# Performance work log

Hardware: AMD Instinct MI355X
Metric: run time of the kernel (lower is better)

Reference implementation:

```python
import jax, jax.numpy as jnp
import numpy as np

GRID_SIZE = 5
SPLINE_ORDER = 3
GRID_RANGE = (-1.0, 1.0)
EPS = 1e-8


def _make_grid():
    h = (GRID_RANGE[1] - GRID_RANGE[0]) / GRID_SIZE
    # knots: [-spline_order, ..., grid_size + spline_order] * h + lo  -> 12 values
    return jnp.arange(-SPLINE_ORDER, GRID_SIZE + SPLINE_ORDER + 1, dtype=jnp.float32) * h + GRID_RANGE[0]


def _bspline_basis(x, grid):
    # x: [N, in]  ->  bases: [N, in, num_basis] with num_basis = grid_size + spline_order
    xe = x[..., None]                                   # [N, in, 1]
    bases = ((xe >= grid[:-1]) & (xe < grid[1:])).astype(x.dtype)  # [N, in, 11]
    for k in range(1, SPLINE_ORDER + 1):
        left = (xe - grid[: -(k + 1)]) / (grid[k:-1] - grid[: -(k + 1)] + EPS) * bases[..., :-1]
        right = (grid[k + 1:] - xe) / (grid[k + 1:] - grid[1:-k] + EPS) * bases[..., 1:]
        bases = left + right
    return bases                                        # [N, in, 8]


def setup_inputs() -> dict:
    key = jax.random.key(0)
    k1, k2, k3 = jax.random.split(key, 3)
    in_f, out_f, num_basis = 1024, 1024, GRID_SIZE + SPLINE_ORDER
    N = 4096
    x = jax.random.normal(k1, (N, in_f), dtype=jnp.float32)
    base_weight = jax.random.normal(k2, (out_f, in_f), dtype=jnp.float32) * (1.0 / np.sqrt(in_f))
    base_bias = jnp.zeros((out_f,), dtype=jnp.float32)
    spline_weight = jax.random.normal(k3, (out_f, in_f, num_basis), dtype=jnp.float32) * (1.0 / np.sqrt(in_f))
    return {"x": x, "base_weight": base_weight, "base_bias": base_bias, "spline_weight": spline_weight}


def reference(x, base_weight, base_bias, spline_weight):
    grid = _make_grid()
    # base path: SiLU(x) @ W_base^T + b
    base_out = jax.nn.silu(x) @ base_weight.T + base_bias          # [N, out]
    # spline path: Cox-de Boor basis then contraction over (in, basis)
    basis = _bspline_basis(x, grid)                                 # [N, in, 8]
    spline_out = jnp.einsum('nib,oib->no', basis, spline_weight)    # [N, out]
    return base_out + spline_out
```

## Files before the change

### kernel.cpp

```cpp
#include <hip/hip_runtime.h>
#include <hip/hip_bf16.h>
#include <stdint.h>

#define IN_F 1024
#define OUT_F 1024
#define NB 8
#define KDIM (IN_F + IN_F * NB)
#define NROWS 4096
#define SLICE_ELEMS (NROWS * OUT_F)
#define PREP_BLOCKS ((NROWS * IN_F) / 256)
#define WCONV_BLOCKS ((OUT_F * KDIM) / (4 * 256))

typedef __attribute__((ext_vector_type(8))) short bf16x8;
typedef __attribute__((ext_vector_type(4))) short bf16x4;
typedef __attribute__((ext_vector_type(4))) float f32x4;

__device__ __forceinline__ void bspline8(float x, float b8[8]) {
  float u = (x + 2.2f) * 2.5f;
  bool in = (u >= 0.0f) && (u < 11.0f);
  float uc = fminf(fmaxf(u, 0.0f), 10.99f);
  int i = (int)uc;
  float f = uc - (float)i;
  float g = 1.0f - f;
  float f2 = f * f, f3 = f2 * f;
  const float s = 1.0f / 6.0f;
  float v0 = f3 * s;
  float v1 = (-3.0f * f3 + 3.0f * f2 + 3.0f * f + 1.0f) * s;
  float v2 = (3.0f * f3 - 6.0f * f2 + 4.0f) * s;
  float v3 = g * g * g * s;
#pragma unroll
  for (int j = 0; j < 8; ++j) {
    int d = i - j;
    float r = (d == 0) ? v0 : (d == 1) ? v1 : (d == 2) ? v2 : (d == 3) ? v3 : 0.0f;
    b8[j] = in ? r : 0.0f;
  }
}

__global__ void prep_all_kernel(const float* __restrict__ x, const float* __restrict__ bw,
                                const float* __restrict__ sw, __hip_bfloat16* __restrict__ A,
                                __hip_bfloat16* __restrict__ W) {
  if (blockIdx.x < PREP_BLOCKS) {
    int idx = blockIdx.x * 256 + threadIdx.x;
    int n = idx >> 10;
    int i = idx & 1023;
    float xv = x[idx];
    float sl = xv / (1.0f + __expf(-xv));
    __hip_bfloat16* row = A + (size_t)n * KDIM;
    row[i] = __float2bfloat16(sl);
    float b8[8];
    bspline8(xv, b8);
    alignas(16) __hip_bfloat16 tmp[8];
#pragma unroll
    for (int c = 0; c < 8; ++c) tmp[c] = __float2bfloat16(b8[c]);
    *(bf16x8*)(row + IN_F + i * 8) = *(const bf16x8*)tmp;
  } else {
    int v = (blockIdx.x - PREP_BLOCKS) * 256 + threadIdx.x;
    int e = v * 4;
    int o = e / KDIM;
    int k = e - o * KDIM;
    float4 val = (k < IN_F) ? *(const float4*)(bw + o * IN_F + k)
                            : *(const float4*)(sw + (size_t)o * (IN_F * NB) + (k - IN_F));
    alignas(8) __hip_bfloat16 t[4];
    t[0] = __float2bfloat16(val.x);
    t[1] = __float2bfloat16(val.y);
    t[2] = __float2bfloat16(val.z);
    t[3] = __float2bfloat16(val.w);
    *(bf16x4*)(W + e) = *(const bf16x4*)t;
  }
}

__global__ __launch_bounds__(512, 2) void gemm8_kernel(const __hip_bfloat16* __restrict__ A,
                                                       const __hip_bfloat16* __restrict__ W,
                                                       float* __restrict__ dst,
                                                       const float* __restrict__ bias,
                                                       int kslice, int use_bias) {
  __shared__ __hip_bfloat16 lA[2][16384];
  __shared__ __hip_bfloat16 lB[2][16384];
  const int tid = threadIdx.x;
  const int wave = tid >> 6;
  const int lane = tid & 63;
  const int warp_m = wave >> 2;
  const int warp_n = wave & 3;
  const int bm = blockIdx.x * 256;
  const int bn = blockIdx.y * 256;
  const int z = blockIdx.z;
  float* __restrict__ d = dst + (size_t)z * SLICE_ELEMS;
  const int kbeg = z * kslice;
  const int NT = kslice >> 6;
  const int NIT = NT >> 1;
  const int srow = lane & 15;
  const int skc = (lane >> 4) * 8;
  const int r = lane & 15;
  const int quad = lane >> 4;

  const __hip_bfloat16* rowA[2];
  const __hip_bfloat16* rowB[2];
  rowA[0] = A + (size_t)(bm + (0 * 8 + wave) * 16 + srow) * KDIM + kbeg + skc;
  rowA[1] = A + (size_t)(bm + (1 * 8 + wave) * 16 + srow) * KDIM + kbeg + skc;
  rowB[0] = W + (size_t)(bn + (0 * 8 + wave) * 16 + srow) * KDIM + kbeg + skc;
  rowB[1] = W + (size_t)(bn + (1 * 8 + wave) * 16 + srow) * KDIM + kbeg + skc;

  f32x4 acc[8][4];
#pragma unroll
  for (int a = 0; a < 8; ++a)
#pragma unroll
    for (int b = 0; b < 4; ++b) acc[a][b] = (f32x4){0.f, 0.f, 0.f, 0.f};

#define GLOAD(SRC, DST)                                                                      \
  __builtin_amdgcn_global_load_lds((const __attribute__((address_space(1))) void*)(SRC),     \
                                   (__attribute__((address_space(3))) void*)(DST), 16, 0, 0)

#define STAGE_HALF(TILE, HID, SLOT)                                              \
  do {                                                                           \
    const int tu_ = (TILE);                                                      \
    const int ts_ = tu_ < NT ? tu_ : NT - 1;                                     \
    if ((HID) < 2) {                                                             \
      const __hip_bfloat16* s_ = rowA[(HID)] + (size_t)ts_ * 64;                 \
      __hip_bfloat16* d_ = &lA[(SLOT)][(((HID) * 8 + wave) * 2 + 0) * 512];      \
      GLOAD(s_, d_);                                                             \
      GLOAD(s_ + 32, d_ + 512);                                                  \
    } else {                                                                     \
      const __hip_bfloat16* s_ = rowB[(HID) - 2] + (size_t)ts_ * 64;             \
      __hip_bfloat16* d_ = &lB[(SLOT)][((((HID) - 2) * 8 + wave) * 2 + 0) * 512];\
      GLOAD(s_, d_);                                                             \
      GLOAD(s_ + 32, d_ + 512);                                                  \
    }                                                                            \
  } while (0)

  bf16x8 a03[4][2], a47[4][2], bfr[4][2];

#define LOAD_A03(SLOT)                                                                      \
  do {                                                                                      \
    _Pragma("unroll") for (int t = 0; t < 4; ++t) {                                         \
      a03[t][0] = *(const bf16x8*)&lA[(SLOT)][((warp_m * 8 + t) * 2 + 0) * 512 + lane * 8]; \
      a03[t][1] = *(const bf16x8*)&lA[(SLOT)][((warp_m * 8 + t) * 2 + 1) * 512 + lane * 8]; \
    }                                                                                       \
  } while (0)
#define LOAD_A47(SLOT)                                                                          \
  do {                                                                                          \
    _Pragma("unroll") for (int t = 0; t < 4; ++t) {                                             \
      a47[t][0] = *(const bf16x8*)&lA[(SLOT)][((warp_m * 8 + 4 + t) * 2 + 0) * 512 + lane * 8]; \
      a47[t][1] = *(const bf16x8*)&lA[(SLOT)][((warp_m * 8 + 4 + t) * 2 + 1) * 512 + lane * 8]; \
    }                                                                                           \
  } while (0)
#define LOAD_B(SLOT)                                                                        \
  do {                                                                                      \
    _Pragma("unroll") for (int u = 0; u < 4; ++u) {                                         \
      bfr[u][0] = *(const bf16x8*)&lB[(SLOT)][((warp_n * 4 + u) * 2 + 0) * 512 + lane * 8]; \
      bfr[u][1] = *(const bf16x8*)&lB[(SLOT)][((warp_n * 4 + u) * 2 + 1) * 512 + lane * 8]; \
    }                                                                                       \
  } while (0)

#define MFMA_QUAD(AF, TM0, TN0)                                                              \
  do {                                                                                       \
    _Pragma("unroll") for (int tm = 0; tm < 4; ++tm)                                         \
    _Pragma("unroll") for (int tn = 0; tn < 2; ++tn)                                         \
    _Pragma("unroll") for (int s = 0; s < 2; ++s)                                            \
        acc[(TM0) + tm][(TN0) + tn] = __builtin_amdgcn_mfma_f32_16x16x32_bf16(               \
            AF[tm][s], bfr[(TN0) + tn][s], acc[(TM0) + tm][(TN0) + tn], 0, 0, 0);            \
  } while (0)

#define PH_BAR_LGKM()                                        \
  do {                                                       \
    __builtin_amdgcn_s_barrier();                            \
    asm volatile("s_waitcnt lgkmcnt(0)" ::: "memory");       \
    __builtin_amdgcn_sched_barrier(0);                       \
  } while (0)
#define PH_BAR()                                             \
  do {                                                       \
    __builtin_amdgcn_s_barrier();                            \
    __builtin_amdgcn_sched_barrier(0);                       \
  } while (0)
#define PH_END()                                             \
  do {                                                       \
    __builtin_amdgcn_s_setprio(0);                           \
    __builtin_amdgcn_sched_barrier(0);                       \
    __builtin_amdgcn_s_barrier();                            \
  } while (0)

  STAGE_HALF(0, 2, 0);
  STAGE_HALF(0, 3, 0);
  STAGE_HALF(0, 0, 0);
  STAGE_HALF(0, 1, 0);
  STAGE_HALF(1, 2, 1);
  STAGE_HALF(1, 3, 1);
  STAGE_HALF(1, 0, 1);
  asm volatile("s_waitcnt vmcnt(6)" ::: "memory");
  __builtin_amdgcn_sched_barrier(0);
  __builtin_amdgcn_s_barrier();

  for (int i = 0; i < NIT; ++i) {
    const int t2 = 2 * i + 2, t3 = 2 * i + 3;
    LOAD_A03(0);
    LOAD_B(0);
    STAGE_HALF(2 * i + 1, 1, 1);
    PH_BAR_LGKM();
    __builtin_amdgcn_s_setprio(1);
    MFMA_QUAD(a03, 0, 0);
    PH_END();
    LOAD_A47(0);
    STAGE_HALF(t2, 2, 0);
    PH_BAR_LGKM();
    __builtin_amdgcn_s_setprio(1);
    MFMA_QUAD(a47, 4, 0);
    PH_END();
    STAGE_HALF(t2, 3, 0);
    PH_BAR();
    __builtin_amdgcn_s_setprio(1);
    MFMA_QUAD(a03, 0, 2);
    PH_END();
    STAGE_HALF(t2, 0, 0);
    asm volatile("s_waitcnt vmcnt(6)" ::: "memory");
    __builtin_amdgcn_sched_barrier(0);
    PH_BAR();
    __builtin_amdgcn_s_setprio(1);
    MFMA_QUAD(a47, 4, 2);
    PH_END();
    LOAD_A03(1);
    LOAD_B(1);
    STAGE_HALF(t2, 1, 0);
    PH_BAR_LGKM();
    __builtin_amdgcn_s_setprio(1);
    MFMA_QUAD(a03, 0, 0);
    PH_END();
    LOAD_A47(1);
    STAGE_HALF(t3, 2, 1);
    PH_BAR_LGKM();
    __builtin_amdgcn_s_setprio(1);
    MFMA_QUAD(a47, 4, 0);
    PH_END();
    STAGE_HALF(t3, 3, 1);
    PH_BAR();
    __builtin_amdgcn_s_setprio(1);
    MFMA_QUAD(a03, 0, 2);
    PH_END();
    STAGE_HALF(t3, 0, 1);
    asm volatile("s_waitcnt vmcnt(6)" ::: "memory");
    __builtin_amdgcn_sched_barrier(0);
    PH_BAR();
    __builtin_amdgcn_s_setprio(1);
    MFMA_QUAD(a47, 4, 2);
    PH_END();
  }
  asm volatile("s_waitcnt vmcnt(0)" ::: "memory");

#undef STAGE_HALF
#undef GLOAD
#undef LOAD_A03
#undef LOAD_A47
#undef LOAD_B
#undef MFMA_QUAD
#undef PH_BAR_LGKM
#undef PH_BAR
#undef PH_END

#pragma unroll
  for (int tm = 0; tm < 8; ++tm) {
#pragma unroll
    for (int tn = 0; tn < 4; ++tn) {
      const int col = bn + warp_n * 64 + tn * 16 + r;
      const float bv = use_bias ? bias[col] : 0.0f;
#pragma unroll
      for (int reg = 0; reg < 4; ++reg) {
        const int rowi = bm + warp_m * 128 + tm * 16 + quad * 4 + reg;
        d[(size_t)rowi * OUT_F + col] = acc[tm][tn][reg] + bv;
      }
    }
  }
}

__global__ void reduce_kernel(const float* __restrict__ P, const float* __restrict__ bias,
                              float* __restrict__ out, int S) {
  int v = blockIdx.x * 256 + threadIdx.x;
  int e = v * 4;
  int o = e & (OUT_F - 1);
  float4 acc = *(const float4*)(bias + o);
  for (int s = 0; s < S; ++s) {
    float4 p = *(const float4*)(P + (size_t)s * SLICE_ELEMS + e);
    acc.x += p.x;
    acc.y += p.y;
    acc.z += p.z;
    acc.w += p.w;
  }
  *(float4*)(out + e) = acc;
}

__global__ void kan_fallback(const float* __restrict__ x, const float* __restrict__ bw,
                             const float* __restrict__ bb, const float* __restrict__ sw,
                             float* __restrict__ out) {
  __shared__ float act[KDIM];
  int n = blockIdx.x;
  for (int i = threadIdx.x; i < IN_F; i += 256) {
    float xv = x[(size_t)n * IN_F + i];
    act[i] = xv / (1.0f + __expf(-xv));
    float b8[8];
    bspline8(xv, b8);
#pragma unroll
    for (int c = 0; c < 8; ++c) act[IN_F + i * 8 + c] = b8[c];
  }
  __syncthreads();
  for (int o = threadIdx.x; o < OUT_F; o += 256) {
    float s = bb[o];
    const float* wbp = bw + (size_t)o * IN_F;
    for (int k = 0; k < IN_F; ++k) s += act[k] * wbp[k];
    const float* wsp = sw + (size_t)o * (IN_F * NB);
    for (int k = 0; k < IN_F * NB; ++k) s += act[IN_F + k] * wsp[k];
    out[(size_t)n * OUT_F + o] = s;
  }
}

extern "C" void kernel_launch(void* const* d_in, const int* in_sizes, int n_in, void* d_out,
                              int out_size, void* d_ws, size_t ws_size, hipStream_t stream) {
  const float* x = (const float*)d_in[0];
  const float* bw = (const float*)d_in[1];
  const float* bb = (const float*)d_in[2];
  const float* sw = (const float*)d_in[3];
  float* out = (float*)d_out;

  const size_t needA = (size_t)NROWS * KDIM * 2;
  const size_t needW = (size_t)OUT_F * KDIM * 2;
  const size_t sliceB = (size_t)SLICE_ELEMS * 4;
  if (ws_size < needA + needW) {
    kan_fallback<<<NROWS, 256, 0, stream>>>(x, bw, bb, sw, out);
    return;
  }
  __hip_bfloat16* A = (__hip_bfloat16*)d_ws;
  __hip_bfloat16* W = (__hip_bfloat16*)((char*)d_ws + needA);
  float* P = (float*)((char*)d_ws + needA + needW);
  const size_t avail = ws_size - needA - needW;
  int S = (avail >= 4 * sliceB) ? 4 : (avail >= 2 * sliceB) ? 2 : 1;

  prep_all_kernel<<<PREP_BLOCKS + WCONV_BLOCKS, 256, 0, stream>>>(x, bw, sw, A, W);
  if (S == 1) {
    gemm8_kernel<<<dim3(NROWS / 256, OUT_F / 256, 1), 512, 0, stream>>>(A, W, out, bb, KDIM, 1);
  } else {
    gemm8_kernel<<<dim3(NROWS / 256, OUT_F / 256, S), 512, 0, stream>>>(A, W, P, bb, KDIM / S, 0);
    reduce_kernel<<<SLICE_ELEMS / (4 * 256), 256, 0, stream>>>(P, bb, out, S);
  }
}
```

Measured before the change: 219.4 us.

## Restructure GEMM main loop to prefetch LDS fragments one phase ahead

After: 244.1 us. +11.3%, slower.

```diff
diff --git a/kernel.cpp b/kernel.cpp
--- a/kernel.cpp
+++ b/kernel.cpp
@@ -87,7 +87,6 @@
   float* __restrict__ d = dst + (size_t)z * SLICE_ELEMS;
   const int kbeg = z * kslice;
   const int NT = kslice >> 6;
-  const int NIT = NT >> 1;
   const int srow = lane & 15;
   const int skc = (lane >> 4) * 8;
   const int r = lane & 15;
@@ -143,12 +142,21 @@
       a47[t][1] = *(const bf16x8*)&lA[(SLOT)][((warp_m * 8 + 4 + t) * 2 + 1) * 512 + lane * 8]; \
     }                                                                                           \
   } while (0)
-#define LOAD_B(SLOT)                                                                        \
+#define LOAD_B01(SLOT)                                                                      \
   do {                                                                                      \
-    _Pragma("unroll") for (int u = 0; u < 4; ++u) {                                         \
+    _Pragma("unroll") for (int u = 0; u < 2; ++u) {                                         \
       bfr[u][0] = *(const bf16x8*)&lB[(SLOT)][((warp_n * 4 + u) * 2 + 0) * 512 + lane * 8]; \
       bfr[u][1] = *(const bf16x8*)&lB[(SLOT)][((warp_n * 4 + u) * 2 + 1) * 512 + lane * 8]; \
     }                                                                                       \
+  } while (0)
+#define LOAD_B23(SLOT)                                                                          \
+  do {                                                                                          \
+    _Pragma("unroll") for (int u = 0; u < 2; ++u) {                                             \
+      bfr[2 + u][0] =                                                                           \
+          *(const bf16x8*)&lB[(SLOT)][((warp_n * 4 + 2 + u) * 2 + 0) * 512 + lane * 8];         \
+      bfr[2 + u][1] =                                                                           \
+          *(const bf16x8*)&lB[(SLOT)][((warp_n * 4 + 2 + u) * 2 + 1) * 512 + lane * 8];         \
+    }                                                                                           \
   } while (0)
 
 #define MFMA_QUAD(AF, TM0, TN0)                                                              \
@@ -160,87 +168,60 @@
             AF[tm][s], bfr[(TN0) + tn][s], acc[(TM0) + tm][(TN0) + tn], 0, 0, 0);            \
   } while (0)
 
-#define PH_BAR_LGKM()                                        \
-  do {                                                       \
-    __builtin_amdgcn_s_barrier();                            \
-    asm volatile("s_waitcnt lgkmcnt(0)" ::: "memory");       \
-    __builtin_amdgcn_sched_barrier(0);                       \
-  } while (0)
-#define PH_BAR()                                             \
-  do {                                                       \
-    __builtin_amdgcn_s_barrier();                            \
-    __builtin_amdgcn_sched_barrier(0);                       \
-  } while (0)
-#define PH_END()                                             \
-  do {                                                       \
-    __builtin_amdgcn_s_setprio(0);                           \
-    __builtin_amdgcn_sched_barrier(0);                       \
-    __builtin_amdgcn_s_barrier();                            \
-  } while (0)
-
+#define PIN() __builtin_amdgcn_sched_barrier(0)
+
+  STAGE_HALF(0, 0, 0);
+  STAGE_HALF(0, 1, 0);
   STAGE_HALF(0, 2, 0);
   STAGE_HALF(0, 3, 0);
-  STAGE_HALF(0, 0, 0);
-  STAGE_HALF(0, 1, 0);
+  STAGE_HALF(1, 0, 1);
+  STAGE_HALF(1, 1, 1);
   STAGE_HALF(1, 2, 1);
   STAGE_HALF(1, 3, 1);
-  STAGE_HALF(1, 0, 1);
-  asm volatile("s_waitcnt vmcnt(6)" ::: "memory");
-  __builtin_amdgcn_sched_barrier(0);
+  asm volatile("s_waitcnt vmcnt(8)" ::: "memory");
+  PIN();
   __builtin_amdgcn_s_barrier();
-
-  for (int i = 0; i < NIT; ++i) {
-    const int t2 = 2 * i + 2, t3 = 2 * i + 3;
-    LOAD_A03(0);
-    LOAD_B(0);
-    STAGE_HALF(2 * i + 1, 1, 1);
-    PH_BAR_LGKM();
+  LOAD_A03(0);
+  LOAD_B01(0);
+  PIN();
+
+  for (int it = 0; it < NT; ++it) {
+    const int p = it & 1;
+    LOAD_A47(p);
+    PIN();
     __builtin_amdgcn_s_setprio(1);
     MFMA_QUAD(a03, 0, 0);
-    PH_END();
-    LOAD_A47(0);
-    STAGE_HALF(t2, 2, 0);
-    PH_BAR_LGKM();
+    __builtin_amdgcn_s_setprio(0);
+    PIN();
+    __builtin_amdgcn_s_barrier();
+    LOAD_B23(p);
+    PIN();
     __builtin_amdgcn_s_setprio(1);
     MFMA_QUAD(a47, 4, 0);
-    PH_END();
-    STAGE_HALF(t2, 3, 0);
-    PH_BAR();
+    __builtin_amdgcn_s_setprio(0);
+    PIN();
+    __builtin_amdgcn_s_barrier();
+    STAGE_HALF(it + 2, 0, p);
+    STAGE_HALF(it + 2, 1, p);
+    PIN();
     __builtin_amdgcn_s_setprio(1);
     MFMA_QUAD(a03, 0, 2);
-    PH_END();
-    STAGE_HALF(t2, 0, 0);
-    asm volatile("s_waitcnt vmcnt(6)" ::: "memory");
-    __builtin_amdgcn_sched_barrier(0);
-    PH_BAR();
+    __builtin_amdgcn_s_setprio(0);
+    PIN();
+    __builtin_amdgcn_s_barrier();
+    STAGE_HALF(it + 2, 2, p);
+    STAGE_HALF(it + 2, 3, p);
+    asm volatile("s_waitcnt vmcnt(8)" ::: "memory");
+    PIN();
+    __builtin_amdgcn_s_barrier();
+    LOAD_A03(p ^ 1);
+    LOAD_B01(p ^ 1);
+    PIN();
     __builtin_amdgcn_s_setprio(1);
     MFMA_QUAD(a47, 4, 2);
-    PH_END();
-    LOAD_A03(1);
-    LOAD_B(1);
-    STAGE_HALF(t2, 1, 0);
-    PH_BAR_LGKM();
-    __builtin_amdgcn_s_setprio(1);
-    MFMA_QUAD(a03, 0, 0);
-    PH_END();
-    LOAD_A47(1);
-    STAGE_HALF(t3, 2, 1);
-    PH_BAR_LGKM();
-    __builtin_amdgcn_s_setprio(1);
-    MFMA_QUAD(a47, 4, 0);
-    PH_END();
-    STAGE_HALF(t3, 3, 1);
-    PH_BAR();
-    __builtin_amdgcn_s_setprio(1);
-    MFMA_QUAD(a03, 0, 2);
-    PH_END();
-    STAGE_HALF(t3, 0, 1);
-    asm volatile("s_waitcnt vmcnt(6)" ::: "memory");
-    __builtin_amdgcn_sched_barrier(0);
-    PH_BAR();
-    __builtin_amdgcn_s_setprio(1);
-    MFMA_QUAD(a47, 4, 2);
-    PH_END();
+    __builtin_amdgcn_s_setprio(0);
+    PIN();
+    __builtin_amdgcn_s_barrier();
   }
   asm volatile("s_waitcnt vmcnt(0)" ::: "memory");
 
@@ -248,11 +229,10 @@
 #undef GLOAD
 #undef LOAD_A03
 #undef LOAD_A47
-#undef LOAD_B
+#undef LOAD_B01
+#undef LOAD_B23
 #undef MFMA_QUAD
-#undef PH_BAR_LGKM
-#undef PH_BAR
-#undef PH_END
+#undef PIN
 
 #pragma unroll
   for (int tm = 0; tm < 8; ++tm) {
```
